# Optimization experiments

Hardware: AMD Instinct MI355X
Metric: run time of the kernel (lower is better)

The kernel has to match this reference:

```python
import jax, jax.numpy as jnp
import numpy as np

N_NODES = 100_000
N_EDGES = 1_600_000
F_NODE = 16
F_EDGE = 8
HID = 128
N_GRAPHS = 2048


def setup_inputs() -> dict:
    key = jax.random.key(0)
    ks = jax.random.split(key, 20)
    inp = {
        "node_attr": jax.random.normal(ks[0], (N_NODES, F_NODE), dtype=jnp.float32),
        "edge_attr": jax.random.normal(ks[1], (N_EDGES, F_EDGE), dtype=jnp.float32),
        "edge_index": jax.random.randint(ks[2], (2, N_EDGES), 0, N_NODES),
        "adj_index": jax.random.randint(ks[3], (2, N_EDGES), 0, N_NODES),
        "adj_value": jax.random.uniform(ks[4], (N_EDGES,), dtype=jnp.float32) * 0.1,
        "batch": jnp.sort(jax.random.randint(ks[5], (N_NODES,), 0, N_GRAPHS)),
    }
    def glorot(k, shape):
        fan_in, fan_out = shape[0], shape[1]
        std = jnp.sqrt(2.0 / (fan_in + fan_out)).astype(jnp.float32)
        return jax.random.normal(k, shape, dtype=jnp.float32) * std
    # attr embedder params
    inp["W_node"] = glorot(ks[6], (F_NODE, HID))
    inp["W_edge"] = glorot(ks[7], (F_EDGE, HID))
    inp["b_embed"] = jnp.zeros((HID,), dtype=jnp.float32)
    # 3 GCN layers
    inp["W1"] = glorot(ks[8], (HID, HID)); inp["b1"] = jnp.zeros((HID,), jnp.float32)
    inp["W2"] = glorot(ks[9], (HID, HID)); inp["b2"] = jnp.zeros((HID,), jnp.float32)
    inp["W3"] = glorot(ks[10], (HID, HID)); inp["b3"] = jnp.zeros((HID,), jnp.float32)
    # predictor MLP
    inp["Wp1"] = glorot(ks[11], (HID, HID)); inp["bp1"] = jnp.full((HID,), 0.01, jnp.float32)
    inp["Wp2"] = glorot(ks[12], (HID, 1));   inp["bp2"] = jnp.full((1,), 0.01, jnp.float32)
    return inp


def _forward(node_attr, edge_attr, adj_value,
             W_node, W_edge, b_embed, W1, b1, W2, b2, W3, b3,
             Wp1, bp1, Wp2, bp2, edge_index, adj_index, batch):
    # --- attr embedder: mix node feats with edge feats scattered to dst nodes ---
    he = edge_attr @ W_edge                                   # [E, H]
    agg = jax.ops.segment_sum(he, edge_index[1], num_segments=N_NODES)
    h = jax.nn.relu(node_attr @ W_node + agg + b_embed)       # [N, H]

    # --- GCN stack: h <- relu(tilde_A @ (h W) + b) via sparse COO SpMM ---
    src, dst = adj_index[0], adj_index[1]
    def gcn(h, W, b):
        hw = h @ W + b                                        # [N, H]
        msg = adj_value[:, None] * hw[dst]                    # [E, H] gather
        return jax.nn.relu(jax.ops.segment_sum(msg, src, num_segments=N_NODES))
    h = gcn(h, W1, b1)
    h = gcn(h, W2, b2)
    h = gcn(h, W3, b3)

    # --- global_add_pool over graphs ---
    fp = jax.ops.segment_sum(h, batch, num_segments=N_GRAPHS)  # [G, H]

    # --- predictor MLP ---
    z = jax.nn.relu(fp @ Wp1 + bp1)
    return z @ Wp2 + bp2                                       # [G, 1]


def reference(node_attr, edge_attr, edge_index, adj_index, adj_value, batch,
              W_node, W_edge, b_embed, W1, b1, W2, b2, W3, b3,
              Wp1, bp1, Wp2, bp2):
    return _forward(node_attr, edge_attr, adj_value,
                    W_node, W_edge, b_embed, W1, b1, W2, b2, W3, b3,
                    Wp1, bp1, Wp2, bp2, edge_index, adj_index, batch)
```

## Files before the change

kernel.cpp:

```cpp
#include <hip/hip_runtime.h>

#define H 128
#define FN 16
#define FE 8
#define NBUK_MAX 1600

__global__ __launch_bounds__(256) void k_hist2(
    const int* __restrict__ k1, const int* __restrict__ k2,
    int* __restrict__ bcnt1, int* __restrict__ bcnt2, int E, int nbuk) {
  __shared__ int h1[NBUK_MAX], h2[NBUK_MAX];
  for (int i = threadIdx.x; i < nbuk; i += 256) { h1[i] = 0; h2[i] = 0; }
  __syncthreads();
  for (int e = blockIdx.x * 256 + threadIdx.x; e < E; e += gridDim.x * 256) {
    atomicAdd(&h1[k1[e] >> 6], 1);
    atomicAdd(&h2[k2[e] >> 6], 1);
  }
  __syncthreads();
  for (int i = threadIdx.x; i < nbuk; i += 256) {
    if (h1[i]) atomicAdd(&bcnt1[i], h1[i]);
    if (h2[i]) atomicAdd(&bcnt2[i], h2[i]);
  }
}

__global__ __launch_bounds__(1024) void k_scan(
    const int* __restrict__ cnt1, int* __restrict__ st1, int* __restrict__ gc1,
    const int* __restrict__ cnt2, int* __restrict__ st2, int* __restrict__ gc2,
    int nbuk) {
  __shared__ int s[1024];
  int tid = threadIdx.x;
  for (int pass = 0; pass < 2; pass++) {
    const int* cnt = pass ? cnt2 : cnt1;
    int* st = pass ? st2 : st1;
    int* gc = pass ? gc2 : gc1;
    int run = 0;
    for (int half = 0; half * 1024 < nbuk; half++) {
      int i = half * 1024 + tid;
      int v = (i < nbuk) ? cnt[i] : 0;
      s[tid] = v; __syncthreads();
      for (int off = 1; off < 1024; off <<= 1) {
        int t = (tid >= off) ? s[tid - off] : 0;
        __syncthreads();
        s[tid] += t;
        __syncthreads();
      }
      int excl = run + s[tid] - v;
      if (i < nbuk) { st[i] = excl; gc[i] = excl; }
      run += s[1023];
      __syncthreads();
    }
    if (tid == 0) st[nbuk] = run;
    __syncthreads();
  }
}

template <int PACKED>
__global__ __launch_bounds__(256) void k_p1_scatter(
    const int* __restrict__ key, const int* __restrict__ dsts,
    const float* __restrict__ vals, int* __restrict__ gcur,
    int* __restrict__ pkey, int2* __restrict__ bpay, int E, int nbuk) {
  __shared__ int hc[NBUK_MAX];
  int tid = threadIdx.x;
  int c0 = blockIdx.x * 8192;
  int c1 = min(c0 + 8192, E);
  for (int i = tid; i < nbuk; i += 256) hc[i] = 0;
  __syncthreads();
  for (int e = c0 + tid; e < c1; e += 256)
    atomicAdd(&hc[key[e] >> 6], 1);
  __syncthreads();
  for (int i = tid; i < nbuk; i += 256) {
    int c = hc[i];
    if (c) hc[i] = atomicAdd(&gcur[i], c);
  }
  __syncthreads();
  for (int e = c0 + tid; e < c1; e += 256) {
    int k = key[e];
    int pos = atomicAdd(&hc[k >> 6], 1);
    if (PACKED) {
      pkey[pos] = (e << 6) | (k & 63);
    } else {
      bpay[pos] = make_int2(dsts[e] | ((k & 63) << 20), __float_as_int(vals[e]));
    }
  }
}

__global__ __launch_bounds__(256) void k_embed_agg(
    const int* __restrict__ pkey, const float* __restrict__ edge_attr,
    const int* __restrict__ bstart, float* __restrict__ agg8, int N) {
  __shared__ float lds[FE][64];
  int b = blockIdx.x, tid = threadIdx.x;
  for (int i = tid; i < FE * 64; i += 256) ((float*)lds)[i] = 0.f;
  __syncthreads();
  int s = bstart[b], t = bstart[b + 1];
  int i = s + tid;
  for (; i + 256 < t; i += 512) {
    int pk0 = pkey[i], pk1 = pkey[i + 256];
    const float4* e0 = (const float4*)(edge_attr + (size_t)(pk0 >> 6) * FE);
    const float4* e1 = (const float4*)(edge_attr + (size_t)(pk1 >> 6) * FE);
    float4 a0 = e0[0], b0 = e0[1], a1 = e1[0], b1 = e1[1];
    int s0 = pk0 & 63, s1 = pk1 & 63;
    atomicAdd(&lds[0][s0], a0.x);  atomicAdd(&lds[1][s0], a0.y);
    atomicAdd(&lds[2][s0], a0.z);  atomicAdd(&lds[3][s0], a0.w);
    atomicAdd(&lds[4][s0], b0.x);  atomicAdd(&lds[5][s0], b0.y);
    atomicAdd(&lds[6][s0], b0.z);  atomicAdd(&lds[7][s0], b0.w);
    atomicAdd(&lds[0][s1], a1.x);  atomicAdd(&lds[1][s1], a1.y);
    atomicAdd(&lds[2][s1], a1.z);  atomicAdd(&lds[3][s1], a1.w);
    atomicAdd(&lds[4][s1], b1.x);  atomicAdd(&lds[5][s1], b1.y);
    atomicAdd(&lds[6][s1], b1.z);  atomicAdd(&lds[7][s1], b1.w);
  }
  for (; i < t; i += 256) {
    int pk = pkey[i];
    int e = pk >> 6, slot = pk & 63;
    const float4* ea = (const float4*)(edge_attr + (size_t)e * FE);
    float4 a = ea[0], b4 = ea[1];
    atomicAdd(&lds[0][slot], a.x);  atomicAdd(&lds[1][slot], a.y);
    atomicAdd(&lds[2][slot], a.z);  atomicAdd(&lds[3][slot], a.w);
    atomicAdd(&lds[4][slot], b4.x); atomicAdd(&lds[5][slot], b4.y);
    atomicAdd(&lds[6][slot], b4.z); atomicAdd(&lds[7][slot], b4.w);
  }
  __syncthreads();
  int node0 = b * 64;
  for (int j = tid; j < 64 * FE; j += 256) {
    int n = node0 + (j >> 3);
    if (n < N) agg8[(size_t)n * FE + (j & 7)] = lds[j & 7][j >> 3];
  }
}

__global__ __launch_bounds__(256) void k_p2(
    const int2* __restrict__ bpay, const int* __restrict__ bstart,
    int* __restrict__ offs, int2* __restrict__ payF, float* __restrict__ rs,
    int N, int E) {
  __shared__ int cnt[64], scn[64], cur[64];
  __shared__ float vsum[64];
  int b = blockIdx.x, tid = threadIdx.x;
  int s = bstart[b], t = bstart[b + 1];
  if (tid < 64) { cnt[tid] = 0; vsum[tid] = 0.f; }
  __syncthreads();
  for (int i = s + tid; i < t; i += 256) atomicAdd(&cnt[(bpay[i].x >> 20) & 63], 1);
  __syncthreads();
  if (tid < 64) scn[tid] = cnt[tid];
  __syncthreads();
  for (int off = 1; off < 64; off <<= 1) {
    int v = 0;
    if (tid < 64 && tid >= off) v = scn[tid - off];
    __syncthreads();
    if (tid < 64 && tid >= off) scn[tid] += v;
    __syncthreads();
  }
  if (tid < 64) {
    int excl = s + scn[tid] - cnt[tid];
    cur[tid] = excl;
    int node = b * 64 + tid;
    if (node < N) offs[node] = excl;
  }
  if (b == 0 && tid == 0) offs[N] = E;
  __syncthreads();
  for (int i = s + tid; i < t; i += 256) {
    int2 p = bpay[i];
    int slot = (p.x >> 20) & 63;
    int pos = atomicAdd(&cur[slot], 1);
    payF[pos] = make_int2(p.x & 0xFFFFF, p.y);
    atomicAdd(&vsum[slot], __int_as_float(p.y));
  }
  __syncthreads();
  if (tid < 64) {
    int node = b * 64 + tid;
    if (node < N) rs[node] = vsum[tid];
  }
}

__global__ __launch_bounds__(256) void k_embed_h(
    const float* __restrict__ node_attr, const float* __restrict__ Wn,
    const float* __restrict__ We8, const float* __restrict__ b,
    const float* __restrict__ agg8, float* __restrict__ h, int N) {
  __shared__ float Ws[FN * H];
  __shared__ float Es[FE * H];
  __shared__ float na[2][FN];
  __shared__ float a8[2][FE];
  for (int i = threadIdx.x; i < FN * H; i += 256) Ws[i] = Wn[i];
  for (int i = threadIdx.x; i < FE * H; i += 256) Es[i] = We8[i];
  int lane = threadIdx.x & 127;
  int sub  = threadIdx.x >> 7;
  for (int n0 = blockIdx.x * 2; n0 < N; n0 += gridDim.x * 2) {
    int n = n0 + sub;
    __syncthreads();
    if (n < N) {
      if (lane < FN) na[sub][lane] = node_attr[(size_t)n * FN + lane];
      else if (lane < FN + FE) a8[sub][lane - FN] = agg8[(size_t)n * FE + (lane - FN)];
    }
    __syncthreads();
    if (n < N) {
      float acc = b[lane];
#pragma unroll
      for (int k = 0; k < FN; k++) acc += na[sub][k] * Ws[k * H + lane];
#pragma unroll
      for (int k = 0; k < FE; k++) acc += a8[sub][k] * Es[k * H + lane];
      h[(size_t)n * H + lane] = fmaxf(acc, 0.f);
    }
  }
}

__global__ __launch_bounds__(256) void k_fused(
    const float* __restrict__ h, const int* __restrict__ offs,
    const int2* __restrict__ pay, const float* __restrict__ W,
    const float* __restrict__ bias, const float* __restrict__ rs,
    float* __restrict__ out, int N) {
  __shared__ float4 hs4[64 * 32];
  int tid = threadIdx.x;
  int c  = tid & 31;
  int rg = tid >> 5;
  int base = blockIdx.x * 64;
  const float4* h4 = (const float4*)h;

  for (int r = 0; r < 8; r++) {
    int row = rg * 8 + r;
    int n = base + row;
    float4 a0 = make_float4(0.f, 0.f, 0.f, 0.f);
    float4 a1 = make_float4(0.f, 0.f, 0.f, 0.f);
    float4 a2 = make_float4(0.f, 0.f, 0.f, 0.f);
    float4 a3 = make_float4(0.f, 0.f, 0.f, 0.f);
    if (n < N) {
      int s = offs[n], t = offs[n + 1];
      int i = s, t4 = s + ((t - s) & ~3);
      for (; i < t4; i += 4) {
        int2 p0 = pay[i], p1 = pay[i + 1], p2 = pay[i + 2], p3 = pay[i + 3];
        float4 h0 = h4[(size_t)p0.x * 32 + c];
        float4 h1 = h4[(size_t)p1.x * 32 + c];
        float4 h2 = h4[(size_t)p2.x * 32 + c];
        float4 h3 = h4[(size_t)p3.x * 32 + c];
        float v0 = __int_as_float(p0.y), v1 = __int_as_float(p1.y);
        float v2 = __int_as_float(p2.y), v3 = __int_as_float(p3.y);
        a0.x += v0 * h0.x; a0.y += v0 * h0.y; a0.z += v0 * h0.z; a0.w += v0 * h0.w;
        a1.x += v1 * h1.x; a1.y += v1 * h1.y; a1.z += v1 * h1.z; a1.w += v1 * h1.w;
        a2.x += v2 * h2.x; a2.y += v2 * h2.y; a2.z += v2 * h2.z; a2.w += v2 * h2.w;
        a3.x += v3 * h3.x; a3.y += v3 * h3.y; a3.z += v3 * h3.z; a3.w += v3 * h3.w;
      }
      for (; i < t; i++) {
        int2 p = pay[i];
        float v = __int_as_float(p.y);
        float4 hv = h4[(size_t)p.x * 32 + c];
        a0.x += v * hv.x; a0.y += v * hv.y; a0.z += v * hv.z; a0.w += v * hv.w;
      }
    }
    hs4[row * 32 + c] = make_float4(a0.x + a1.x + a2.x + a3.x,
                                    a0.y + a1.y + a2.y + a3.y,
                                    a0.z + a1.z + a2.z + a3.z,
                                    a0.w + a1.w + a2.w + a3.w);
  }
  __syncthreads();

  const float4* W4 = (const float4*)W;
  float4 acc[8];
#pragma unroll
  for (int i = 0; i < 8; i++) acc[i] = make_float4(0.f, 0.f, 0.f, 0.f);
#pragma unroll 2
  for (int k = 0; k < 32; k++) {
    float4 w0 = W4[(k * 4 + 0) * 32 + c];
    float4 w1 = W4[(k * 4 + 1) * 32 + c];
    float4 w2 = W4[(k * 4 + 2) * 32 + c];
    float4 w3 = W4[(k * 4 + 3) * 32 + c];
#pragma unroll
    for (int i = 0; i < 8; i++) {
      float4 hv = hs4[(rg + 8 * i) * 32 + k];
      acc[i].x += hv.x * w0.x + hv.y * w1.x + hv.z * w2.x + hv.w * w3.x;
      acc[i].y += hv.x * w0.y + hv.y * w1.y + hv.z * w2.y + hv.w * w3.y;
      acc[i].z += hv.x * w0.z + hv.y * w1.z + hv.z * w2.z + hv.w * w3.z;
      acc[i].w += hv.x * w0.w + hv.y * w1.w + hv.z * w2.w + hv.w * w3.w;
    }
  }

  float4 bv = ((const float4*)bias)[c];
#pragma unroll
  for (int i = 0; i < 8; i++) {
    int row = rg + 8 * i;
    int n = base + row;
    if (n < N) {
      float rsv = rs[n];
      float4 o;
      o.x = fmaxf(acc[i].x + rsv * bv.x, 0.f);
      o.y = fmaxf(acc[i].y + rsv * bv.y, 0.f);
      o.z = fmaxf(acc[i].z + rsv * bv.z, 0.f);
      o.w = fmaxf(acc[i].w + rsv * bv.w, 0.f);
      ((float4*)out)[(size_t)n * 32 + c] = o;
    }
  }
}

template <int RELU_OUT>
__global__ __launch_bounds__(256) void k_gemm(
    const float* __restrict__ in, const float* __restrict__ W,
    const float* __restrict__ bias, float* __restrict__ out, int N) {
  __shared__ float4 hs4[64 * 32];
  int tid = threadIdx.x;
  int c  = tid & 31;
  int rg = tid >> 5;
  int rowBase = blockIdx.x * 64;
  const float4* in4 = (const float4*)in;
  const float4* W4  = (const float4*)W;
#pragma unroll
  for (int j = 0; j < 8; j++) {
    int q = tid + 256 * j;
    int r = rowBase + (q >> 5);
    int rr = (r < N) ? r : (N - 1);
    hs4[q] = in4[(size_t)rr * 32 + (q & 31)];
  }
  __syncthreads();
  float4 acc[8];
#pragma unroll
  for (int i = 0; i < 8; i++) acc[i] = make_float4(0.f, 0.f, 0.f, 0.f);
#pragma unroll 2
  for (int k = 0; k < 32; k++) {
    float4 w0 = W4[(k * 4 + 0) * 32 + c];
    float4 w1 = W4[(k * 4 + 1) * 32 + c];
    float4 w2 = W4[(k * 4 + 2) * 32 + c];
    float4 w3 = W4[(k * 4 + 3) * 32 + c];
#pragma unroll
    for (int i = 0; i < 8; i++) {
      float4 hv = hs4[(rg + 8 * i) * 32 + k];
      acc[i].x += hv.x * w0.x + hv.y * w1.x + hv.z * w2.x + hv.w * w3.x;
      acc[i].y += hv.x * w0.y + hv.y * w1.y + hv.z * w2.y + hv.w * w3.y;
      acc[i].z += hv.x * w0.z + hv.y * w1.z + hv.z * w2.z + hv.w * w3.z;
      acc[i].w += hv.x * w0.w + hv.y * w1.w + hv.z * w2.w + hv.w * w3.w;
    }
  }
  float4 bv = ((const float4*)bias)[c];
#pragma unroll
  for (int i = 0; i < 8; i++) {
    int row = rowBase + rg + 8 * i;
    if (row < N) {
      float4 o = make_float4(acc[i].x + bv.x, acc[i].y + bv.y,
                             acc[i].z + bv.z, acc[i].w + bv.w);
      if (RELU_OUT) {
        o.x = fmaxf(o.x, 0.f); o.y = fmaxf(o.y, 0.f);
        o.z = fmaxf(o.z, 0.f); o.w = fmaxf(o.w, 0.f);
      }
      ((float4*)out)[(size_t)row * 32 + c] = o;
    }
  }
}

__global__ __launch_bounds__(256) void k_gbounds(
    const int* __restrict__ batch, int* __restrict__ gstart, int N, int G) {
  int n = blockIdx.x * 256 + threadIdx.x;
  if (n > N) return;
  if (n == 0) {
    for (int g = 0; g <= batch[0]; g++) gstart[g] = 0;
  } else if (n == N) {
    for (int g = batch[N - 1] + 1; g <= G; g++) gstart[g] = N;
  } else {
    int b0 = batch[n - 1], b1 = batch[n];
    for (int g = b0 + 1; g <= b1; g++) gstart[g] = n;
  }
}

__global__ __launch_bounds__(128) void k_pool_seg(
    const float* __restrict__ h, const int* __restrict__ gstart,
    float* __restrict__ fp, int G) {
  int g = blockIdx.x;
  int j = threadIdx.x;
  int s = gstart[g], t = gstart[g + 1];
  float acc = 0.f;
  for (int n = s; n < t; n++) acc += h[(size_t)n * H + j];
  fp[(size_t)g * H + j] = acc;
}

__global__ __launch_bounds__(256) void k_pred2(
    const float* __restrict__ z, const float* __restrict__ Wp2,
    const float* __restrict__ bp2, float* __restrict__ out, int G) {
  int g = blockIdx.x * 4 + (threadIdx.x >> 6);
  if (g >= G) return;
  int l = threadIdx.x & 63;
  float2 zv = ((const float2*)z)[(size_t)g * 64 + l];
  float2 wv = ((const float2*)Wp2)[l];
  float v = zv.x * wv.x + zv.y * wv.y;
#pragma unroll
  for (int off = 32; off > 0; off >>= 1) v += __shfl_down(v, off, 64);
  if (l == 0) out[g] = v + bp2[0];
}

extern "C" void kernel_launch(void* const* d_in, const int* in_sizes, int n_in,
                              void* d_out, int out_size, void* d_ws, size_t ws_size,
                              hipStream_t stream) {
  const float* node_attr  = (const float*)d_in[0];
  const float* edge_attr  = (const float*)d_in[1];
  const int*   edge_index = (const int*)d_in[2];
  const int*   adj_index  = (const int*)d_in[3];
  const float* adj_value  = (const float*)d_in[4];
  const int*   batch      = (const int*)d_in[5];
  const float* W_node  = (const float*)d_in[6];
  const float* W_edge  = (const float*)d_in[7];
  const float* b_embed = (const float*)d_in[8];
  const float* W1 = (const float*)d_in[9];
  const float* b1 = (const float*)d_in[10];
  const float* W2 = (const float*)d_in[11];
  const float* b2 = (const float*)d_in[12];
  const float* W3 = (const float*)d_in[13];
  const float* b3 = (const float*)d_in[14];
  const float* Wp1 = (const float*)d_in[15];
  const float* bp1 = (const float*)d_in[16];
  const float* Wp2 = (const float*)d_in[17];
  const float* bp2 = (const float*)d_in[18];
  float* out = (float*)d_out;

  const int E = in_sizes[4];
  const int N = in_sizes[5];
  const int G = out_size;
  const int nbuk = (N + 63) >> 6;
  const int p1b = (E + 8191) / 8192;

  float* A     = (float*)d_ws;
  float* B     = A + (size_t)N * H;
  int2*  payF  = (int2*)(B + (size_t)N * H);
  float* fpool = (float*)(payF + E);
  int*   bcnt1 = (int*)(fpool + (size_t)G * H);
  int*   bcnt2 = bcnt1 + nbuk;
  int*   bst1  = bcnt2 + nbuk;
  int*   gcur1 = bst1 + nbuk + 1;
  int*   bst2  = gcur1 + nbuk;
  int*   gcur2 = bst2 + nbuk + 1;
  int*   offs2 = gcur2 + nbuk;
  int*   gstart= offs2 + N + 1;
  float* rs    = (float*)(gstart + G + 1);
  float* agg8  = A;
  int*   pkey  = (int*)B;
  int2*  bpay2 = (int2*)(((int*)B) + E);
  float* zbuf  = B;

  hipMemsetAsync(bcnt1, 0, (size_t)2 * nbuk * sizeof(int), stream);
  k_hist2<<<512, 256, 0, stream>>>(edge_index + E, adj_index, bcnt1, bcnt2, E, nbuk);
  k_scan<<<1, 1024, 0, stream>>>(bcnt1, bst1, gcur1, bcnt2, bst2, gcur2, nbuk);

  k_p1_scatter<1><<<p1b, 256, 0, stream>>>(edge_index + E, nullptr, nullptr,
                                           gcur1, pkey, nullptr, E, nbuk);
  k_p1_scatter<0><<<p1b, 256, 0, stream>>>(adj_index, adj_index + E, adj_value,
                                           gcur2, nullptr, bpay2, E, nbuk);

  k_embed_agg<<<nbuk, 256, 0, stream>>>(pkey, edge_attr, bst1, agg8, N);
  k_p2<<<nbuk, 256, 0, stream>>>(bpay2, bst2, offs2, payF, rs, N, E);

  k_embed_h<<<4096, 256, 0, stream>>>(node_attr, W_node, W_edge, b_embed, agg8, B, N);

  k_gbounds<<<(N + 256) / 256, 256, 0, stream>>>(batch, gstart, N, G);

  int lb = (N + 63) / 64;
  k_fused<<<lb, 256, 0, stream>>>(B, offs2, payF, W1, b1, rs, A, N);
  k_fused<<<lb, 256, 0, stream>>>(A, offs2, payF, W2, b2, rs, B, N);
  k_fused<<<lb, 256, 0, stream>>>(B, offs2, payF, W3, b3, rs, A, N);

  k_pool_seg<<<G, 128, 0, stream>>>(A, gstart, fpool, G);
  k_gemm<1><<<(G + 63) / 64, 256, 0, stream>>>(fpool, Wp1, bp1, zbuf, G);
  k_pred2<<<(G + 3) / 4, 256, 0, stream>>>(zbuf, Wp2, bp2, out, G);
}
```

Before: 948.6 us.

## Merge preprocessing kernels, widen GCN blocks, fuse predictor head and parallelize pooling

Folds graph-bounds computation into the histogram kernel, merges the two scatter passes and the two per-bucket passes into single launches, and fuses the predictor's second layer into the first GEMM with a warp reduction. The fused GCN kernel moves to 512-thread blocks, with each thread handling 4 rows instead of 8. Pooling now uses 8 row groups with float4 loads and a shared-memory reduction. The aim is fewer launches and more parallelism in the GCN and pooling stages, at the cost of higher register and occupancy pressure in k_fused.

```diff
diff --git a/kernel.cpp b/kernel.cpp
--- a/kernel.cpp
+++ b/kernel.cpp
@@ -5,13 +5,27 @@
 #define FE 8
 #define NBUK_MAX 1600
 
-__global__ __launch_bounds__(256) void k_hist2(
+__global__ __launch_bounds__(256) void k_hist2_gb(
     const int* __restrict__ k1, const int* __restrict__ k2,
-    int* __restrict__ bcnt1, int* __restrict__ bcnt2, int E, int nbuk) {
+    int* __restrict__ bcnt1, int* __restrict__ bcnt2, int E, int nbuk,
+    const int* __restrict__ batch, int* __restrict__ gstart, int N, int G) {
+  if (blockIdx.x >= 512) {
+    int n = (blockIdx.x - 512) * 256 + threadIdx.x;
+    if (n > N) return;
+    if (n == 0) {
+      for (int g = 0; g <= batch[0]; g++) gstart[g] = 0;
+    } else if (n == N) {
+      for (int g = batch[N - 1] + 1; g <= G; g++) gstart[g] = N;
+    } else {
+      int b0 = batch[n - 1], b1 = batch[n];
+      for (int g = b0 + 1; g <= b1; g++) gstart[g] = n;
+    }
+    return;
+  }
   __shared__ int h1[NBUK_MAX], h2[NBUK_MAX];
   for (int i = threadIdx.x; i < nbuk; i += 256) { h1[i] = 0; h2[i] = 0; }
   __syncthreads();
-  for (int e = blockIdx.x * 256 + threadIdx.x; e < E; e += gridDim.x * 256) {
+  for (int e = blockIdx.x * 256 + threadIdx.x; e < E; e += 512 * 256) {
     atomicAdd(&h1[k1[e] >> 6], 1);
     atomicAdd(&h2[k2[e] >> 6], 1);
   }
@@ -53,14 +67,17 @@
   }
 }
 
-template <int PACKED>
-__global__ __launch_bounds__(256) void k_p1_scatter(
-    const int* __restrict__ key, const int* __restrict__ dsts,
-    const float* __restrict__ vals, int* __restrict__ gcur,
-    int* __restrict__ pkey, int2* __restrict__ bpay, int E, int nbuk) {
+__global__ __launch_bounds__(256) void k_p1_both(
+    const int* __restrict__ k1, const int* __restrict__ adj, const float* __restrict__ vals,
+    int* __restrict__ gcur1, int* __restrict__ gcur2,
+    int* __restrict__ pkey, int2* __restrict__ bpay, int E, int nbuk, int p1b) {
   __shared__ int hc[NBUK_MAX];
   int tid = threadIdx.x;
-  int c0 = blockIdx.x * 8192;
+  bool packed = (int)blockIdx.x < p1b;
+  int chunk = packed ? blockIdx.x : blockIdx.x - p1b;
+  const int* key = packed ? k1 : adj;
+  int* gcur = packed ? gcur1 : gcur2;
+  int c0 = chunk * 8192;
   int c1 = min(c0 + 8192, E);
   for (int i = tid; i < nbuk; i += 256) hc[i] = 0;
   __syncthreads();
@@ -72,99 +89,106 @@
     if (c) hc[i] = atomicAdd(&gcur[i], c);
   }
   __syncthreads();
-  for (int e = c0 + tid; e < c1; e += 256) {
-    int k = key[e];
-    int pos = atomicAdd(&hc[k >> 6], 1);
-    if (PACKED) {
+  if (packed) {
+    for (int e = c0 + tid; e < c1; e += 256) {
+      int k = key[e];
+      int pos = atomicAdd(&hc[k >> 6], 1);
       pkey[pos] = (e << 6) | (k & 63);
-    } else {
+    }
+  } else {
+    const int* dsts = adj + E;
+    for (int e = c0 + tid; e < c1; e += 256) {
+      int k = key[e];
+      int pos = atomicAdd(&hc[k >> 6], 1);
       bpay[pos] = make_int2(dsts[e] | ((k & 63) << 20), __float_as_int(vals[e]));
     }
   }
 }
 
-__global__ __launch_bounds__(256) void k_embed_agg(
+__global__ __launch_bounds__(256) void k_agg_p2(
     const int* __restrict__ pkey, const float* __restrict__ edge_attr,
-    const int* __restrict__ bstart, float* __restrict__ agg8, int N) {
+    const int* __restrict__ bst1, float* __restrict__ agg8,
+    const int2* __restrict__ bpay, const int* __restrict__ bst2,
+    int* __restrict__ offs, int2* __restrict__ payF, float* __restrict__ rs,
+    int N, int E, int nbuk) {
   __shared__ float lds[FE][64];
-  int b = blockIdx.x, tid = threadIdx.x;
-  for (int i = tid; i < FE * 64; i += 256) ((float*)lds)[i] = 0.f;
-  __syncthreads();
-  int s = bstart[b], t = bstart[b + 1];
-  int i = s + tid;
-  for (; i + 256 < t; i += 512) {
-    int pk0 = pkey[i], pk1 = pkey[i + 256];
-    const float4* e0 = (const float4*)(edge_attr + (size_t)(pk0 >> 6) * FE);
-    const float4* e1 = (const float4*)(edge_attr + (size_t)(pk1 >> 6) * FE);
-    float4 a0 = e0[0], b0 = e0[1], a1 = e1[0], b1 = e1[1];
-    int s0 = pk0 & 63, s1 = pk1 & 63;
-    atomicAdd(&lds[0][s0], a0.x);  atomicAdd(&lds[1][s0], a0.y);
-    atomicAdd(&lds[2][s0], a0.z);  atomicAdd(&lds[3][s0], a0.w);
-    atomicAdd(&lds[4][s0], b0.x);  atomicAdd(&lds[5][s0], b0.y);
-    atomicAdd(&lds[6][s0], b0.z);  atomicAdd(&lds[7][s0], b0.w);
-    atomicAdd(&lds[0][s1], a1.x);  atomicAdd(&lds[1][s1], a1.y);
-    atomicAdd(&lds[2][s1], a1.z);  atomicAdd(&lds[3][s1], a1.w);
-    atomicAdd(&lds[4][s1], b1.x);  atomicAdd(&lds[5][s1], b1.y);
-    atomicAdd(&lds[6][s1], b1.z);  atomicAdd(&lds[7][s1], b1.w);
-  }
-  for (; i < t; i += 256) {
-    int pk = pkey[i];
-    int e = pk >> 6, slot = pk & 63;
-    const float4* ea = (const float4*)(edge_attr + (size_t)e * FE);
-    float4 a = ea[0], b4 = ea[1];
-    atomicAdd(&lds[0][slot], a.x);  atomicAdd(&lds[1][slot], a.y);
-    atomicAdd(&lds[2][slot], a.z);  atomicAdd(&lds[3][slot], a.w);
-    atomicAdd(&lds[4][slot], b4.x); atomicAdd(&lds[5][slot], b4.y);
-    atomicAdd(&lds[6][slot], b4.z); atomicAdd(&lds[7][slot], b4.w);
-  }
-  __syncthreads();
-  int node0 = b * 64;
-  for (int j = tid; j < 64 * FE; j += 256) {
-    int n = node0 + (j >> 3);
-    if (n < N) agg8[(size_t)n * FE + (j & 7)] = lds[j & 7][j >> 3];
-  }
-}
-
-__global__ __launch_bounds__(256) void k_p2(
-    const int2* __restrict__ bpay, const int* __restrict__ bstart,
-    int* __restrict__ offs, int2* __restrict__ payF, float* __restrict__ rs,
-    int N, int E) {
   __shared__ int cnt[64], scn[64], cur[64];
   __shared__ float vsum[64];
-  int b = blockIdx.x, tid = threadIdx.x;
-  int s = bstart[b], t = bstart[b + 1];
-  if (tid < 64) { cnt[tid] = 0; vsum[tid] = 0.f; }
-  __syncthreads();
-  for (int i = s + tid; i < t; i += 256) atomicAdd(&cnt[(bpay[i].x >> 20) & 63], 1);
-  __syncthreads();
-  if (tid < 64) scn[tid] = cnt[tid];
-  __syncthreads();
-  for (int off = 1; off < 64; off <<= 1) {
-    int v = 0;
-    if (tid < 64 && tid >= off) v = scn[tid - off];
-    __syncthreads();
-    if (tid < 64 && tid >= off) scn[tid] += v;
-    __syncthreads();
-  }
-  if (tid < 64) {
-    int excl = s + scn[tid] - cnt[tid];
-    cur[tid] = excl;
-    int node = b * 64 + tid;
-    if (node < N) offs[node] = excl;
-  }
-  if (b == 0 && tid == 0) offs[N] = E;
-  __syncthreads();
-  for (int i = s + tid; i < t; i += 256) {
-    int2 p = bpay[i];
-    int slot = (p.x >> 20) & 63;
-    int pos = atomicAdd(&cur[slot], 1);
-    payF[pos] = make_int2(p.x & 0xFFFFF, p.y);
-    atomicAdd(&vsum[slot], __int_as_float(p.y));
-  }
-  __syncthreads();
-  if (tid < 64) {
-    int node = b * 64 + tid;
-    if (node < N) rs[node] = vsum[tid];
+  int tid = threadIdx.x;
+
+  if ((int)blockIdx.x < nbuk) {
+    int b = blockIdx.x;
+    for (int i = tid; i < FE * 64; i += 256) ((float*)lds)[i] = 0.f;
+    __syncthreads();
+    int s = bst1[b], t = bst1[b + 1];
+    int i = s + tid;
+    for (; i + 256 < t; i += 512) {
+      int pk0 = pkey[i], pk1 = pkey[i + 256];
+      const float4* e0 = (const float4*)(edge_attr + (size_t)(pk0 >> 6) * FE);
+      const float4* e1 = (const float4*)(edge_attr + (size_t)(pk1 >> 6) * FE);
+      float4 a0 = e0[0], b0 = e0[1], a1 = e1[0], b1 = e1[1];
+      int s0 = pk0 & 63, s1 = pk1 & 63;
+      atomicAdd(&lds[0][s0], a0.x);  atomicAdd(&lds[1][s0], a0.y);
+      atomicAdd(&lds[2][s0], a0.z);  atomicAdd(&lds[3][s0], a0.w);
+      atomicAdd(&lds[4][s0], b0.x);  atomicAdd(&lds[5][s0], b0.y);
+      atomicAdd(&lds[6][s0], b0.z);  atomicAdd(&lds[7][s0], b0.w);
+      atomicAdd(&lds[0][s1], a1.x);  atomicAdd(&lds[1][s1], a1.y);
+      atomicAdd(&lds[2][s1], a1.z);  atomicAdd(&lds[3][s1], a1.w);
+      atomicAdd(&lds[4][s1], b1.x);  atomicAdd(&lds[5][s1], b1.y);
+      atomicAdd(&lds[6][s1], b1.z);  atomicAdd(&lds[7][s1], b1.w);
+    }
+    for (; i < t; i += 256) {
+      int pk = pkey[i];
+      int e = pk >> 6, slot = pk & 63;
+      const float4* ea = (const float4*)(edge_attr + (size_t)e * FE);
+      float4 a = ea[0], b4 = ea[1];
+      atomicAdd(&lds[0][slot], a.x);  atomicAdd(&lds[1][slot], a.y);
+      atomicAdd(&lds[2][slot], a.z);  atomicAdd(&lds[3][slot], a.w);
+      atomicAdd(&lds[4][slot], b4.x); atomicAdd(&lds[5][slot], b4.y);
+      atomicAdd(&lds[6][slot], b4.z); atomicAdd(&lds[7][slot], b4.w);
+    }
+    __syncthreads();
+    int node0 = b * 64;
+    for (int j = tid; j < 64 * FE; j += 256) {
+      int n = node0 + (j >> 3);
+      if (n < N) agg8[(size_t)n * FE + (j & 7)] = lds[j & 7][j >> 3];
+    }
+  } else {
+    int b = blockIdx.x - nbuk;
+    int s = bst2[b], t = bst2[b + 1];
+    if (tid < 64) { cnt[tid] = 0; vsum[tid] = 0.f; }
+    __syncthreads();
+    for (int i = s + tid; i < t; i += 256) atomicAdd(&cnt[(bpay[i].x >> 20) & 63], 1);
+    __syncthreads();
+    if (tid < 64) scn[tid] = cnt[tid];
+    __syncthreads();
+    for (int off = 1; off < 64; off <<= 1) {
+      int v = 0;
+      if (tid < 64 && tid >= off) v = scn[tid - off];
+      __syncthreads();
+      if (tid < 64 && tid >= off) scn[tid] += v;
+      __syncthreads();
+    }
+    if (tid < 64) {
+      int excl = s + scn[tid] - cnt[tid];
+      cur[tid] = excl;
+      int node = b * 64 + tid;
+      if (node < N) offs[node] = excl;
+    }
+    if (b == 0 && tid == 0) offs[N] = E;
+    __syncthreads();
+    for (int i = s + tid; i < t; i += 256) {
+      int2 p = bpay[i];
+      int slot = (p.x >> 20) & 63;
+      int pos = atomicAdd(&cur[slot], 1);
+      payF[pos] = make_int2(p.x & 0xFFFFF, p.y);
+      atomicAdd(&vsum[slot], __int_as_float(p.y));
+    }
+    __syncthreads();
+    if (tid < 64) {
+      int node = b * 64 + tid;
+      if (node < N) rs[node] = vsum[tid];
+    }
   }
 }
 
@@ -199,7 +223,7 @@
   }
 }
 
-__global__ __launch_bounds__(256) void k_fused(
+__global__ __launch_bounds__(512, 8) void k_fused(
     const float* __restrict__ h, const int* __restrict__ offs,
     const int2* __restrict__ pay, const float* __restrict__ W,
     const float* __restrict__ bias, const float* __restrict__ rs,
@@ -211,8 +235,8 @@
   int base = blockIdx.x * 64;
   const float4* h4 = (const float4*)h;
 
-  for (int r = 0; r < 8; r++) {
-    int row = rg * 8 + r;
+  for (int r = 0; r < 4; r++) {
+    int row = rg * 4 + r;
     int n = base + row;
     float4 a0 = make_float4(0.f, 0.f, 0.f, 0.f);
     float4 a1 = make_float4(0.f, 0.f, 0.f, 0.f);
@@ -249,9 +273,9 @@
   __syncthreads();
 
   const float4* W4 = (const float4*)W;
-  float4 acc[8];
-#pragma unroll
-  for (int i = 0; i < 8; i++) acc[i] = make_float4(0.f, 0.f, 0.f, 0.f);
+  float4 acc[4];
+#pragma unroll
+  for (int i = 0; i < 4; i++) acc[i] = make_float4(0.f, 0.f, 0.f, 0.f);
 #pragma unroll 2
   for (int k = 0; k < 32; k++) {
     float4 w0 = W4[(k * 4 + 0) * 32 + c];
@@ -259,8 +283,8 @@
     float4 w2 = W4[(k * 4 + 2) * 32 + c];
     float4 w3 = W4[(k * 4 + 3) * 32 + c];
 #pragma unroll
-    for (int i = 0; i < 8; i++) {
-      float4 hv = hs4[(rg + 8 * i) * 32 + k];
+    for (int i = 0; i < 4; i++) {
+      float4 hv = hs4[(rg + 16 * i) * 32 + k];
       acc[i].x += hv.x * w0.x + hv.y * w1.x + hv.z * w2.x + hv.w * w3.x;
       acc[i].y += hv.x * w0.y + hv.y * w1.y + hv.z * w2.y + hv.w * w3.y;
       acc[i].z += hv.x * w0.z + hv.y * w1.z + hv.z * w2.z + hv.w * w3.z;
@@ -270,8 +294,8 @@
 
   float4 bv = ((const float4*)bias)[c];
 #pragma unroll
-  for (int i = 0; i < 8; i++) {
-    int row = rg + 8 * i;
+  for (int i = 0; i < 4; i++) {
+    int row = rg + 16 * i;
     int n = base + row;
     if (n < N) {
       float rsv = rs[n];
@@ -285,10 +309,10 @@
   }
 }
 
-template <int RELU_OUT>
-__global__ __launch_bounds__(256) void k_gemm(
+__global__ __launch_bounds__(256) void k_gemm_pred(
     const float* __restrict__ in, const float* __restrict__ W,
-    const float* __restrict__ bias, float* __restrict__ out, int N) {
+    const float* __restrict__ bias, const float* __restrict__ Wp2,
+    const float* __restrict__ bp2, float* __restrict__ out, int N) {
   __shared__ float4 hs4[64 * 32];
   int tid = threadIdx.x;
   int c  = tid & 31;
@@ -323,58 +347,47 @@
     }
   }
   float4 bv = ((const float4*)bias)[c];
+  float4 wp = ((const float4*)Wp2)[c];
+  float bp = bp2[0];
 #pragma unroll
   for (int i = 0; i < 8; i++) {
     int row = rowBase + rg + 8 * i;
-    if (row < N) {
-      float4 o = make_float4(acc[i].x + bv.x, acc[i].y + bv.y,
-                             acc[i].z + bv.z, acc[i].w + bv.w);
-      if (RELU_OUT) {
-        o.x = fmaxf(o.x, 0.f); o.y = fmaxf(o.y, 0.f);
-        o.z = fmaxf(o.z, 0.f); o.w = fmaxf(o.w, 0.f);
-      }
-      ((float4*)out)[(size_t)row * 32 + c] = o;
-    }
-  }
-}
-
-__global__ __launch_bounds__(256) void k_gbounds(
-    const int* __restrict__ batch, int* __restrict__ gstart, int N, int G) {
-  int n = blockIdx.x * 256 + threadIdx.x;
-  if (n > N) return;
-  if (n == 0) {
-    for (int g = 0; g <= batch[0]; g++) gstart[g] = 0;
-  } else if (n == N) {
-    for (int g = batch[N - 1] + 1; g <= G; g++) gstart[g] = N;
-  } else {
-    int b0 = batch[n - 1], b1 = batch[n];
-    for (int g = b0 + 1; g <= b1; g++) gstart[g] = n;
-  }
-}
-
-__global__ __launch_bounds__(128) void k_pool_seg(
+    float4 o;
+    o.x = fmaxf(acc[i].x + bv.x, 0.f);
+    o.y = fmaxf(acc[i].y + bv.y, 0.f);
+    o.z = fmaxf(acc[i].z + bv.z, 0.f);
+    o.w = fmaxf(acc[i].w + bv.w, 0.f);
+    float v = o.x * wp.x + o.y * wp.y + o.z * wp.z + o.w * wp.w;
+#pragma unroll
+    for (int off = 16; off > 0; off >>= 1) v += __shfl_down(v, off, 32);
+    if (c == 0 && row < N) out[row] = v + bp;
+  }
+}
+
+__global__ __launch_bounds__(256) void k_pool_seg(
     const float* __restrict__ h, const int* __restrict__ gstart,
     float* __restrict__ fp, int G) {
+  __shared__ float4 red[8][32];
   int g = blockIdx.x;
-  int j = threadIdx.x;
+  int c = threadIdx.x & 31, rg = threadIdx.x >> 5;
   int s = gstart[g], t = gstart[g + 1];
-  float acc = 0.f;
-  for (int n = s; n < t; n++) acc += h[(size_t)n * H + j];
-  fp[(size_t)g * H + j] = acc;
-}
-
-__global__ __launch_bounds__(256) void k_pred2(
-    const float* __restrict__ z, const float* __restrict__ Wp2,
-    const float* __restrict__ bp2, float* __restrict__ out, int G) {
-  int g = blockIdx.x * 4 + (threadIdx.x >> 6);
-  if (g >= G) return;
-  int l = threadIdx.x & 63;
-  float2 zv = ((const float2*)z)[(size_t)g * 64 + l];
-  float2 wv = ((const float2*)Wp2)[l];
-  float v = zv.x * wv.x + zv.y * wv.y;
-#pragma unroll
-  for (int off = 32; off > 0; off >>= 1) v += __shfl_down(v, off, 64);
-  if (l == 0) out[g] = v + bp2[0];
+  const float4* h4 = (const float4*)h;
+  float4 a = make_float4(0.f, 0.f, 0.f, 0.f);
+  for (int n = s + rg; n < t; n += 8) {
+    float4 v = h4[(size_t)n * 32 + c];
+    a.x += v.x; a.y += v.y; a.z += v.z; a.w += v.w;
+  }
+  red[rg][c] = a;
+  __syncthreads();
+  if (rg == 0) {
+    float4 r = red[0][c];
+#pragma unroll
+    for (int j = 1; j < 8; j++) {
+      float4 v = red[j][c];
+      r.x += v.x; r.y += v.y; r.z += v.z; r.w += v.w;
+    }
+    ((float4*)fp)[(size_t)g * 32 + c] = r;
+  }
 }
 
 extern "C" void kernel_launch(void* const* d_in, const int* in_sizes, int n_in,
@@ -406,6 +419,7 @@
   const int G = out_size;
   const int nbuk = (N + 63) >> 6;
   const int p1b = (E + 8191) / 8192;
+  const int gbB = (N + 256) / 256;
 
   float* A     = (float*)d_ws;
   float* B     = A + (size_t)N * H;
@@ -423,30 +437,25 @@
   float* agg8  = A;
   int*   pkey  = (int*)B;
   int2*  bpay2 = (int2*)(((int*)B) + E);
-  float* zbuf  = B;
 
   hipMemsetAsync(bcnt1, 0, (size_t)2 * nbuk * sizeof(int), stream);
-  k_hist2<<<512, 256, 0, stream>>>(edge_index + E, adj_index, bcnt1, bcnt2, E, nbuk);
+  k_hist2_gb<<<512 + gbB, 256, 0, stream>>>(edge_index + E, adj_index, bcnt1, bcnt2,
+                                            E, nbuk, batch, gstart, N, G);
   k_scan<<<1, 1024, 0, stream>>>(bcnt1, bst1, gcur1, bcnt2, bst2, gcur2, nbuk);
 
-  k_p1_scatter<1><<<p1b, 256, 0, stream>>>(edge_index + E, nullptr, nullptr,
-                                           gcur1, pkey, nullptr, E, nbuk);
-  k_p1_scatter<0><<<p1b, 256, 0, stream>>>(adj_index, adj_index + E, adj_value,
-                                           gcur2, nullptr, bpay2, E, nbuk);
-
-  k_embed_agg<<<nbuk, 256, 0, stream>>>(pkey, edge_attr, bst1, agg8, N);
-  k_p2<<<nbuk, 256, 0, stream>>>(bpay2, bst2, offs2, payF, rs, N, E);
+  k_p1_both<<<2 * p1b, 256, 0, stream>>>(edge_index + E, adj_index, adj_value,
+                                         gcur1, gcur2, pkey, bpay2, E, nbuk, p1b);
+
+  k_agg_p2<<<2 * nbuk, 256, 0, stream>>>(pkey, edge_attr, bst1, agg8,
+                                         bpay2, bst2, offs2, payF, rs, N, E, nbuk);
 
   k_embed_h<<<4096, 256, 0, stream>>>(node_attr, W_node, W_edge, b_embed, agg8, B, N);
 
-  k_gbounds<<<(N + 256) / 256, 256, 0, stream>>>(batch, gstart, N, G);
-
   int lb = (N + 63) / 64;
-  k_fused<<<lb, 256, 0, stream>>>(B, offs2, payF, W1, b1, rs, A, N);
-  k_fused<<<lb, 256, 0, stream>>>(A, offs2, payF, W2, b2, rs, B, N);
-  k_fused<<<lb, 256, 0, stream>>>(B, offs2, payF, W3, b3, rs, A, N);
-
-  k_pool_seg<<<G, 128, 0, stream>>>(A, gstart, fpool, G);
-  k_gemm<1><<<(G + 63) / 64, 256, 0, stream>>>(fpool, Wp1, bp1, zbuf, G);
-  k_pred2<<<(G + 3) / 4, 256, 0, stream>>>(zbuf, Wp2, bp2, out, G);
-}
+  k_fused<<<lb, 512, 0, stream>>>(B, offs2, payF, W1, b1, rs, A, N);
+  k_fused<<<lb, 512, 0, stream>>>(A, offs2, payF, W2, b2, rs, B, N);
+  k_fused<<<lb, 512, 0, stream>>>(B, offs2, payF, W3, b3, rs, A, N);
+
+  k_pool_seg<<<G, 256, 0, stream>>>(A, gstart, fpool, G);
+  k_gemm_pred<<<(G + 63) / 64, 256, 0, stream>>>(fpool, Wp1, bp1, Wp2, bp2, out, G);
+}
```

Measured after the change: 955.1 us. No clear change (+0.7%).
